# Performance work log

Measured on AMD Instinct MI355X. Metric: run time of the kernel, lower is better.

The kernel has to match this reference:

```python
import jax, jax.numpy as jnp
import numpy as np
from functools import partial

TAU = 2.0
BN_EPS = 1e-5
SG_ALPHA = 4.0  # spikingjelly surrogate.Sigmoid default

@jax.custom_vjp
def heaviside(x):
    return (x >= 0.0).astype(x.dtype)

def _heaviside_fwd(x):
    return heaviside(x), x

def _heaviside_bwd(x, g):
    s = jax.nn.sigmoid(SG_ALPHA * x)
    return (g * SG_ALPHA * s * (1.0 - s),)

heaviside.defvjp(_heaviside_fwd, _heaviside_bwd)

def lif(x_seq, v_threshold=1.0):
    # MultiStepLIFNode: tau=2, decay_input=True, v_reset=0 (hard reset), detach_reset
    def step(v, x):
        v = v + (x - v) / TAU
        s = heaviside(v - v_threshold)
        v = v * (1.0 - jax.lax.stop_gradient(s))
        return v, s
    _, s_seq = jax.lax.scan(step, jnp.zeros_like(x_seq[0]), x_seq)
    return s_seq

def conv1x1_bn(x, w, gamma, beta, mean, var, b=None):
    # x: [T,B,C,N]; w: [Cout,Cin]; 1x1 conv == channel matmul; BN in eval mode
    y = jnp.einsum('oc,tbcn->tbon', w, x)
    if b is not None:
        y = y + b[:, None]
    inv = gamma / jnp.sqrt(var + BN_EPS)
    return y * inv[:, None] + (beta - mean * inv)[:, None]

def setup_inputs() -> dict:
    key = jax.random.key(0)
    ks = jax.random.split(key, 24)
    T, B, C, N = 4, 32, 384, 196
    d = {}
    d['x'] = jax.random.normal(ks[0], (T, B, C, N), dtype=jnp.float32)
    d['policy'] = jax.random.uniform(ks[1], (T * B, N, 1), dtype=jnp.float32)
    scale = 1.0 / np.sqrt(C)
    for i, p in enumerate(['q', 'k', 'v', 'proj']):
        base = 2 + i * 5
        d[p + '_w'] = jax.random.normal(ks[base], (C, C), dtype=jnp.float32) * scale
        d[p + '_gamma'] = jnp.ones((C,), jnp.float32)
        d[p + '_beta'] = jnp.zeros((C,), jnp.float32)
        d[p + '_mean'] = jax.random.normal(ks[base + 1], (C,), dtype=jnp.float32) * 0.1
        d[p + '_var'] = jax.random.uniform(ks[base + 2], (C,), dtype=jnp.float32, minval=0.5, maxval=1.5)
    d['proj_b'] = jnp.zeros((C,), jnp.float32)
    return d

def _to_heads(s, H):
    T, B, C, N = s.shape
    # [T,B,C,N] -> [T,B,N,H,D] -> [T,B,H,N,D]
    return s.transpose(0, 1, 3, 2).reshape(T, B, N, H, C // H).transpose(0, 1, 3, 2, 4)

def reference(x, policy, q_w, q_gamma, q_beta, q_mean, q_var,
              k_w, k_gamma, k_beta, k_mean, k_var,
              v_w, v_gamma, v_beta, v_mean, v_var,
              proj_w, proj_gamma, proj_beta, proj_mean, proj_var, proj_b):
    T, B, C, N = x.shape
    H = 12
    attn_scale = 0.25
    q = _to_heads(lif(conv1x1_bn(x, q_w, q_gamma, q_beta, q_mean, q_var)), H)
    k = _to_heads(lif(conv1x1_bn(x, k_w, k_gamma, k_beta, k_mean, k_var)), H)
    v = _to_heads(lif(conv1x1_bn(x, v_w, v_gamma, v_beta, v_mean, v_var)), H)
    attn = jnp.einsum('tbhnd,tbhmd->tbhnm', q, k)
    # attention_policy: attn *= (policy + (1-policy)*eye)
    pol = policy.reshape(T, B, 1, 1, N)
    eye = jnp.eye(N, dtype=attn.dtype)
    attn = attn * (pol + (1.0 - pol) * eye)
    y = jnp.einsum('tbhnm,tbhmd->tbhnd', attn, v) * attn_scale
    y = y.transpose(0, 1, 2, 4, 3).reshape(T, B, C, N)
    y = lif(y, v_threshold=0.5)
    y = conv1x1_bn(y, proj_w, proj_gamma, proj_beta, proj_mean, proj_var, b=proj_b)
    return lif(y)
```

## Files before the change

### kernel.cpp

```cpp
#include <hip/hip_runtime.h>

typedef unsigned int u32;
typedef __bf16 bf16x8 __attribute__((ext_vector_type(8)));
typedef __bf16 bf16x4v __attribute__((ext_vector_type(4)));
typedef _Float16 f16x8 __attribute__((ext_vector_type(8)));
typedef float f32x4 __attribute__((ext_vector_type(4)));

#define Tn 4
#define Bn 32
#define Cn 384
#define Nn 196
#define Hn 12
#define CNn (Cn*Nn)
#define BCNn (Bn*CNn)
#define BHNn (Bn*Hn*Nn)
#define PBITS (Tn*BHNn)
#define TBCNn (Tn*BCNn)
#define NCOLS 6272
#define WSZ 147456

__device__ __forceinline__ void split3(float v, __bf16& h, __bf16& m, __bf16& l) {
  h = (__bf16)v;  float r = v - (float)h;
  m = (__bf16)r;  float r2 = r - (float)m;
  l = (__bf16)r2;
}
__device__ __forceinline__ void split2h(float v, _Float16& h, _Float16& l) {
  h = (_Float16)v;  l = (_Float16)(v - (float)h);
}

__device__ __forceinline__ void gl_lds16(const void* g, void* l) {
  __builtin_amdgcn_global_load_lds(
      (const __attribute__((address_space(1))) unsigned int*)g,
      (__attribute__((address_space(3))) unsigned int*)l, 16, 0, 0);
}

struct WSplitArgs {
  const float* w[4]; const float* g[4]; const float* be[4];
  const float* mu[4]; const float* va[4]; const float* bias;
};
__global__ __launch_bounds__(256) void prep(
    WSplitArgs a, _Float16* __restrict__ wsp16, __bf16* __restrict__ wspb,
    float* __restrict__ shv, const float* __restrict__ x,
    _Float16* __restrict__ xs) {
  __shared__ float tile[49 * 130];
  const int bx = blockIdx.x;
  const int tid = threadIdx.x;
  if (bx < 2304) {
    const int i = bx * 256 + tid;
    const int p = i / WSZ, r = i - p * WSZ;
    const int o = r / Cn, cc = r - o * Cn;
    const float iv = a.g[p][o] / sqrtf(a.va[p][o] + 1e-5f);
    const float wv = a.w[p][r] * iv;
    const int toff = ((o >> 4) * 12 + (cc >> 5)) * 512 +
                     (((cc >> 3) & 3) << 7) + ((o & 15) << 3) + (cc & 7);
    if (p < 3) {
      _Float16 h, l;
      split2h(wv, h, l);
      wsp16[(size_t)(p * 2 + 0) * WSZ + toff] = h;
      wsp16[(size_t)(p * 2 + 1) * WSZ + toff] = l;
    } else {
      __bf16 h, m, l;
      split3(wv, h, m, l);
      wspb[(size_t)0 * WSZ + toff] = h;
      wspb[(size_t)1 * WSZ + toff] = m;
      wspb[(size_t)2 * WSZ + toff] = l;
    }
    if (cc == 0) {
      float sh = a.be[p][o] - a.mu[p][o] * iv;
      if (p == 3) sh += a.bias[o] * iv;
      shv[p * Cn + o] = sh;
    }
    return;
  }
  const int bid2 = bx - 2304;
  const int t = bid2 & 3, b = (bid2 >> 2) & 31, zz = bid2 >> 7;
  const int ct = zz >> 2, nch = zz & 3;
  const int c0 = ct * 128, n0 = nch * 49;
  for (int idx = tid; idx < 49 * 128; idx += 256) {
    const int n = idx % 49, c = idx / 49;
    tile[n * 130 + c] = x[(size_t)t * BCNn + (size_t)b * CNn +
                          (size_t)(c0 + c) * Nn + n0 + n];
  }
  __syncthreads();
  for (int idx = tid; idx < 49 * 64; idx += 256) {
    const int cp = idx & 63, n = idx >> 6;
    const float v0 = tile[n * 130 + cp * 2];
    const float v1 = tile[n * 130 + cp * 2 + 1];
    _Float16 h0, l0, h1, l1;
    split2h(v0, h0, l0);
    split2h(v1, h1, l1);
    const size_t col = (size_t)t * NCOLS + (size_t)b * Nn + n0 + n;
    union { _Float16 f[2]; u32 u; } uh, ul;
    uh.f[0] = h0; uh.f[1] = h1;
    ul.f[0] = l0; ul.f[1] = l1;
    ((u32*)(xs + col * Cn + c0))[cp] = uh.u;
    ((u32*)(xs + (size_t)TBCNn + col * Cn + c0))[cp] = ul.u;
  }
}

__global__ __launch_bounds__(256, 2) void gemm_qkv_lif(
    const _Float16* __restrict__ xs,
    const _Float16* __restrict__ wsp16,
    const float* __restrict__ shv,
    u32* __restrict__ bq, u32* __restrict__ bk, u32* __restrict__ bv)
{
  __shared__ _Float16 Bsw[5][2][64][32];
  const int orig = blockIdx.x;
  const int xcd = orig & 7, i8 = orig >> 3;
  const int wgid = xcd * 110 + (xcd < 2 ? xcd : 2) + i8;
  const int colt = wgid / 9, v = wgid - colt * 9;
  const int col0 = colt * 64;
  const int p = v / 3, mt = v - p * 3;
  const int o0 = mt * 128;
  const int tid = threadIdx.x, lane = tid & 63, wid = tid >> 6;
  const int wm = wid >> 1, wn = wid & 1;
  const int quad = lane >> 4, nl = lane & 15;
  u32* __restrict__ bits = (p == 0) ? bq : (p == 1) ? bk : bv;

  u32 afOff[2][4];
#pragma unroll
  for (int s = 0; s < 2; ++s)
#pragma unroll
    for (int mi = 0; mi < 4; ++mi)
      afOff[s][mi] = (u32)((((p * 2 + s) * WSZ) +
                            (mt * 8 + wm * 4 + mi) * 6144) * 2) +
                     (u32)(lane * 16);
  u32 bOff[2];
#pragma unroll
  for (int i = 0; i < 2; ++i) {
    const int c = i * 256 + wid * 64 + lane;
    const int s = c >> 8, rem = c & 255, row = rem >> 2, kb = rem & 3;
    const int kbs = kb ^ ((row >> 1) & 3);
    bOff[i] = (u32)(((size_t)s * TBCNn + (size_t)(col0 + row) * Cn + kbs * 8) * 2);
  }
  const char* wB = (const char*)wsp16;
  const char* xB = (const char*)xs;
  char* bD0 = (char*)&Bsw[0][0][0][0] + wid * 1024;

#define STAGE_B(g_) do {                                                   \
    const int t_ = ((g_) / 24) * 2 + ((g_) & 1);                           \
    const int kk_ = (((g_) % 24) >> 1);                                    \
    const u32 bk_ = (u32)(kk_ * 64) + (u32)t_ * (u32)(NCOLS * Cn * 2);     \
    char* d_ = bD0 + ((g_) % 5) * 8192;                                    \
    _Pragma("unroll") for (int i_ = 0; i_ < 2; ++i_)                       \
      gl_lds16(xB + bOff[i_] + bk_, d_ + i_ * 4096);                       \
  } while (0)
#define LOAD_AF(DST, g_) do {                                              \
    const u32 ak2_ = (u32)(((g_) % 12) * 1024);                            \
    _Pragma("unroll") for (int s_ = 0; s_ < 2; ++s_)                       \
    _Pragma("unroll") for (int m_ = 0; m_ < 4; ++m_)                       \
      DST[s_][m_] = *(const f16x8*)(wB + afOff[s_][m_] + ak2_);            \
  } while (0)

  f32x4 sh_[4];
#pragma unroll
  for (int mi = 0; mi < 4; ++mi)
    sh_[mi] = *(const f32x4*)&shv[p * Cn + o0 + wm * 64 + mi * 16 + quad * 4];

  f32x4 acc0[4][2], acc1[4][2];
  f32x4 vst[4][2] = {};
  f16x8 afA[2][4], afB[2][4];

  auto epi = [&](f32x4 (&ac)[4][2], int t) {
#pragma unroll
    for (int ni = 0; ni < 2; ++ni) {
      u32 w0 = 0, w1 = 0;
#pragma unroll
      for (int mi = 0; mi < 4; ++mi) {
#pragma unroll
        for (int r = 0; r < 4; ++r) {
          const float y = ac[mi][ni][r] + sh_[mi][r];
          const float vv = vst[mi][ni][r];
          const float nv = vv + (y - vv) * 0.5f;
          const bool sk = nv >= 1.0f;
          vst[mi][ni][r] = sk ? 0.f : nv;
          const u32 b1 = sk ? 1u : 0u;
          const int pos = ((mi & 1) << 4) + (quad << 2) + r;
          if (mi < 2) w0 |= b1 << pos; else w1 |= b1 << pos;
        }
      }
      w0 |= __shfl_xor(w0, 16); w0 |= __shfl_xor(w0, 32);
      w1 |= __shfl_xor(w1, 16); w1 |= __shfl_xor(w1, 32);
      if (quad == 0) {
        const int col = col0 + wn * 32 + ni * 16 + nl;
        const int bb = col / Nn, nn = col - bb * Nn;
        u32* bp = bits + (size_t)t * BHNn +
                  ((size_t)bb * Hn + (mt * 4 + wm * 2)) * Nn + nn;
        bp[0] = w0;
        bp[Nn] = w1;
      }
    }
  };

  auto sub = [&](f16x8 (&afc)[2][4], f16x8 (&afn)[2][4], int g) {
    const int kk = g % 12;
    const int be = (2 * g) % 5, bo = (2 * g + 1) % 5;
    if (g == 0)       asm volatile("s_waitcnt vmcnt(14)" ::: "memory");
    else if (g == 23) asm volatile("s_waitcnt vmcnt(18)" ::: "memory");
    else              asm volatile("s_waitcnt vmcnt(22)" ::: "memory");
    __builtin_amdgcn_s_barrier();
    __builtin_amdgcn_sched_barrier(0);
    if (g < 22) STAGE_B(2 * g + 4);
    __builtin_amdgcn_sched_barrier(0);
    if (kk == 0) {
#pragma unroll
      for (int mi = 0; mi < 4; ++mi)
#pragma unroll
        for (int ni = 0; ni < 2; ++ni) {
          acc0[mi][ni] = f32x4{0.f, 0.f, 0.f, 0.f};
          acc1[mi][ni] = f32x4{0.f, 0.f, 0.f, 0.f};
        }
    }
    {
      f16x8 bfr[2][2];
#pragma unroll
      for (int i = 0; i < 2; ++i) {
        const int rb = wn * 32 + i * 16 + nl;
        const int kb2 = (quad ^ ((rb >> 1) & 3)) * 8;
        bfr[0][i] = *(const f16x8*)&Bsw[be][0][rb][kb2];
        bfr[1][i] = *(const f16x8*)&Bsw[be][1][rb][kb2];
      }
      __builtin_amdgcn_s_setprio(1);
#pragma unroll
      for (int mi = 0; mi < 4; ++mi)
#pragma unroll
        for (int ni = 0; ni < 2; ++ni) {
          f32x4 c = acc0[mi][ni];
          c = __builtin_amdgcn_mfma_f32_16x16x32_f16(afc[0][mi], bfr[0][ni], c, 0, 0, 0);
          c = __builtin_amdgcn_mfma_f32_16x16x32_f16(afc[0][mi], bfr[1][ni], c, 0, 0, 0);
          c = __builtin_amdgcn_mfma_f32_16x16x32_f16(afc[1][mi], bfr[0][ni], c, 0, 0, 0);
          acc0[mi][ni] = c;
        }
      __builtin_amdgcn_s_setprio(0);
    }
    if (g == 22)      asm volatile("s_waitcnt vmcnt(12)" ::: "memory");
    else if (g == 23) asm volatile("s_waitcnt vmcnt(8)"  ::: "memory");
    else              asm volatile("s_waitcnt vmcnt(14)" ::: "memory");
    __builtin_amdgcn_s_barrier();
    __builtin_amdgcn_sched_barrier(0);
    if (g < 23) LOAD_AF(afn, g + 1);
    __builtin_amdgcn_sched_barrier(0);
    if (g < 22) STAGE_B(2 * g + 5);
    __builtin_amdgcn_sched_barrier(0);
    {
      f16x8 bfr[2][2];
#pragma unroll
      for (int i = 0; i < 2; ++i) {
        const int rb = wn * 32 + i * 16 + nl;
        const int kb2 = (quad ^ ((rb >> 1) & 3)) * 8;
        bfr[0][i] = *(const f16x8*)&Bsw[bo][0][rb][kb2];
        bfr[1][i] = *(const f16x8*)&Bsw[bo][1][rb][kb2];
      }
      __builtin_amdgcn_s_setprio(1);
#pragma unroll
      for (int mi = 0; mi < 4; ++mi)
#pragma unroll
        for (int ni = 0; ni < 2; ++ni) {
          f32x4 c = acc1[mi][ni];
          c = __builtin_amdgcn_mfma_f32_16x16x32_f16(afc[0][mi], bfr[0][ni], c, 0, 0, 0);
          c = __builtin_amdgcn_mfma_f32_16x16x32_f16(afc[0][mi], bfr[1][ni], c, 0, 0, 0);
          c = __builtin_amdgcn_mfma_f32_16x16x32_f16(afc[1][mi], bfr[0][ni], c, 0, 0, 0);
          acc1[mi][ni] = c;
        }
      __builtin_amdgcn_s_setprio(0);
    }
    if (kk == 11) {
      const int p2 = g / 12;
      epi(acc0, p2 * 2 + 0);
      epi(acc1, p2 * 2 + 1);
    }
  };

  STAGE_B(0); STAGE_B(1); STAGE_B(2);
  LOAD_AF(afA, 0);
  STAGE_B(3);

#pragma unroll 1
  for (int gp = 0; gp < 12; ++gp) {
    sub(afA, afB, 2 * gp);
    sub(afB, afA, 2 * gp + 1);
  }
#undef STAGE_B
#undef LOAD_AF
}

#define USTR 232
#define GSTR 40
__global__ __launch_bounds__(256, 2) void attn_lif(
    const u32* __restrict__ qb, const u32* __restrict__ kb,
    const u32* __restrict__ vb, const float* __restrict__ policy,
    __bf16* __restrict__ sp) {
  __shared__ u32 qs[208], ks[224], vs_[224];
  __shared__ float ps[224];
  __shared__ __bf16 psp[3][224];
  __shared__ __bf16 Ul[3][32][USTR];
  __shared__ __bf16 GT[3][32][GSTR];
  const int bh = blockIdx.x;
  const int bN = bh / Hn;
  const int h = bh - bN * Hn;
  const int tid = threadIdx.x;
  const int lane = tid & 63, wid = tid >> 6;
  const int quad = lane >> 4, nl = lane & 15;
  const int wm1 = wid >> 1, wn1 = wid & 1;
  const __bf16 one = (__bf16)1.0f, zero = (__bf16)0.0f;

  float vst[4][2][4] = {};

  for (int t = 0; t < Tn; ++t) {
    const int tb = t * Bn + bN;
    const int gid = tb * Hn + h;
    if (t) __syncthreads();
    for (int i = tid; i < 224; i += 256) {
      const bool in = i < Nn;
      if (i < 208) qs[i] = in ? qb[(size_t)gid * Nn + i] : 0u;
      ks[i] = in ? kb[(size_t)gid * Nn + i] : 0u;
      vs_[i] = in ? vb[(size_t)gid * Nn + i] : 0u;
      const float p = in ? policy[(size_t)tb * Nn + i] : 0.f;
      ps[i] = p;
      __bf16 hh, mm, ll;
      split3(p, hh, mm, ll);
      psp[0][i] = hh; psp[1][i] = mm; psp[2][i] = ll;
    }
    __syncthreads();

#pragma unroll
    for (int it = 0; it < 7; ++it) {
      const int idx = tid + it * 256;
      const int d = idx & 31, mg = idx >> 5;
      __bf16 u4[3][4];
#pragma unroll
      for (int j = 0; j < 4; ++j) {
        const int m = mg * 4 + j;
        const bool bit = (vs_[m] >> d) & 1u;
#pragma unroll
        for (int s = 0; s < 3; ++s)
          u4[s][j] = bit ? psp[s][m] : zero;
      }
#pragma unroll
      for (int s = 0; s < 3; ++s)
        *(bf16x4v*)&Ul[s][d][mg * 4] = *(bf16x4v*)u4[s];
    }
    __syncthreads();

    f32x4 gacc = {0.f, 0.f, 0.f, 0.f};
    const int crow = wm1 * 16 + nl;
    const int drow = wn1 * 16 + nl;
#pragma unroll
    for (int slab = 0; slab < 7; ++slab) {
      const int m0 = slab * 32 + quad * 8;
      u32 kw[8];
      *(uint4*)&kw[0] = *(const uint4*)&ks[m0];
      *(uint4*)&kw[4] = *(const uint4*)&ks[m0 + 4];
      __bf16 a8[8];
#pragma unroll
      for (int j = 0; j < 8; ++j)
        a8[j] = ((kw[j] >> crow) & 1u) ? one : zero;
      const bf16x8 af = *(const bf16x8*)a8;
#pragma unroll
      for (int s = 0; s < 3; ++s)
        gacc = __builtin_amdgcn_mfma_f32_16x16x32_bf16(
            af, *(const bf16x8*)&Ul[s][drow][slab * 32 + quad * 8], gacc, 0, 0, 0);
    }
#pragma unroll
    for (int r = 0; r < 4; ++r) {
      __bf16 gh, gm, gl;
      split3(gacc[r], gh, gm, gl);
      const int cc = wm1 * 16 + quad * 4 + r;
      GT[0][drow][cc] = gh;
      GT[1][drow][cc] = gm;
      GT[2][drow][cc] = gl;
    }
    __syncthreads();

    bf16x8 bfr2[3][2];
#pragma unroll
    for (int s = 0; s < 3; ++s)
#pragma unroll
      for (int nt = 0; nt < 2; ++nt)
        bfr2[s][nt] = *(const bf16x8*)&GT[s][nt * 16 + nl][quad * 8];

    f32x4 acc2[4][2] = {};
#pragma unroll
    for (int mi = 0; mi < 4; ++mi) {
      const int lt = wid + mi * 4;
      if (lt < 13) {
        const u32 qw = qs[lt * 16 + nl];
        __bf16 a8[8];
#pragma unroll
        for (int j = 0; j < 8; ++j)
          a8[j] = ((qw >> (quad * 8 + j)) & 1u) ? one : zero;
        const bf16x8 af2 = *(const bf16x8*)a8;
#pragma unroll
        for (int nt = 0; nt < 2; ++nt) {
          f32x4 c = acc2[mi][nt];
          c = __builtin_amdgcn_mfma_f32_16x16x32_bf16(af2, bfr2[0][nt], c, 0, 0, 0);
          c = __builtin_amdgcn_mfma_f32_16x16x32_bf16(af2, bfr2[1][nt], c, 0, 0, 0);
          c = __builtin_amdgcn_mfma_f32_16x16x32_bf16(af2, bfr2[2][nt], c, 0, 0, 0);
          acc2[mi][nt] = c;
        }
      }
    }
#pragma unroll
    for (int mi = 0; mi < 4; ++mi) {
      const int lt = wid + mi * 4;
      if (lt >= 13) continue;
#pragma unroll
      for (int r = 0; r < 4; ++r) {
        const int n = lt * 16 + quad * 4 + r;
        if (n >= Nn) continue;
        const float ann = (float)__popc(qs[n] & ks[n]);
        const float wd = ann * (1.0f - ps[n]);
        const u32 vn = vs_[n];
        __bf16* op = sp + (size_t)t * BCNn + ((size_t)bN * Nn + n) * Cn + h * 32;
#pragma unroll
        for (int nt = 0; nt < 2; ++nt) {
          const int d = nt * 16 + nl;
          const float bit = (float)((vn >> d) & 1u);
          const float y = (acc2[mi][nt][r] + wd * bit) * 0.25f;
          const float vv = vst[mi][nt][r];
          const float nv = vv + (y - vv) * 0.5f;
          const bool s = nv >= 0.5f;
          vst[mi][nt][r] = s ? 0.f : nv;
          op[d] = (__bf16)(s ? 1.0f : 0.0f);
        }
      }
    }
  }
}

__global__ __launch_bounds__(256, 3) void gemm_proj_lif(
    const __bf16* __restrict__ sp, const __bf16* __restrict__ wspb,
    const float* __restrict__ shv, float* __restrict__ out)
{
  __shared__ __bf16 Bsw[5][64][32];
  const int orig = blockIdx.x;
  const int xcd = orig & 7, i8 = orig >> 3;
  const int wgid = xcd * 73 + (xcd < 4 ? xcd : 4) + i8;
  const int colt = wgid / 6, ot = wgid - colt * 6;
  const int col0 = colt * 64;
  const int o0 = ot * 64;
  const int tid = threadIdx.x, lane = tid & 63, wid = tid >> 6;
  const int wm = wid >> 1, wn = wid & 1;
  const int quad = lane >> 4, nl = lane & 15;

  u32 afOff[3][2];
#pragma unroll
  for (int s = 0; s < 3; ++s)
#pragma unroll
    for (int mi = 0; mi < 2; ++mi)
      afOff[s][mi] = (u32)(((s * WSZ) + (ot * 4 + wm * 2 + mi) * 6144) * 2) +
                     (u32)(lane * 16);
  u32 bOff;
  {
    const int c = wid * 64 + lane;
    const int row = c >> 2, kb = c & 3;
    const int kbs = kb ^ ((row >> 1) & 3);
    bOff = (u32)(((size_t)(col0 + row) * Cn + kbs * 8) * 2);
  }
  const char* wB = (const char*)wspb;
  const char* sB = (const char*)sp;
  char* bD0 = (char*)&Bsw[0][0][0] + wid * 1024;

#define STAGE_B(g_) do {                                                   \
    const int t_ = ((g_) / 24) * 2 + ((g_) & 1);                           \
    const int kk_ = (((g_) % 24) >> 1);                                    \
    const u32 bk_ = (u32)(kk_ * 64) + (u32)t_ * (u32)(BCNn * 2);           \
    gl_lds16(sB + bOff + bk_, bD0 + ((g_) % 5) * 4096);                    \
  } while (0)
#define LOAD_AF(DST, g_) do {                                              \
    const u32 ak2_ = (u32)(((g_) % 12) * 1024);                            \
    _Pragma("unroll") for (int s_ = 0; s_ < 3; ++s_)                       \
    _Pragma("unroll") for (int m_ = 0; m_ < 2; ++m_)                       \
      DST[s_][m_] = *(const bf16x8*)(wB + afOff[s_][m_] + ak2_);           \
  } while (0)

  f32x4 sh_[2];
#pragma unroll
  for (int mi = 0; mi < 2; ++mi)
    sh_[mi] = *(const f32x4*)&shv[3 * Cn + o0 + wm * 32 + mi * 16 + quad * 4];

  f32x4 acc0[2][2], acc1[2][2];
  f32x4 vst[2][2] = {};
  bf16x8 afA[3][2], afB[3][2];

  auto epi = [&](f32x4 (&ac)[2][2], int t) {
#pragma unroll
    for (int mi = 0; mi < 2; ++mi) {
      const int ob = o0 + wm * 32 + mi * 16 + quad * 4;
#pragma unroll
      for (int ni = 0; ni < 2; ++ni) {
        const int col = col0 + wn * 32 + ni * 16 + nl;
        const int bb = col / Nn, nn = col - bb * Nn;
        float* op = out + (size_t)t * BCNn + (size_t)bb * CNn + nn;
#pragma unroll
        for (int r = 0; r < 4; ++r) {
          const float y = ac[mi][ni][r] + sh_[mi][r];
          const float vv = vst[mi][ni][r];
          const float nv = vv + (y - vv) * 0.5f;
          const bool sk = nv >= 1.0f;
          vst[mi][ni][r] = sk ? 0.f : nv;
          op[(size_t)(ob + r) * Nn] = sk ? 1.0f : 0.0f;
        }
      }
    }
  };

  auto sub = [&](bf16x8 (&afc)[3][2], bf16x8 (&afn)[3][2], int g) {
    const int kk = g % 12;
    const int be = (2 * g) % 5, bo = (2 * g + 1) % 5;
    if (g == 23) asm volatile("s_waitcnt vmcnt(0)" ::: "memory");
    else         asm volatile("s_waitcnt vmcnt(1)" ::: "memory");
    __builtin_amdgcn_s_barrier();
    __builtin_amdgcn_sched_barrier(0);
    if (g < 22) STAGE_B(2 * g + 4);
    __builtin_amdgcn_sched_barrier(0);
    if (kk == 0) {
#pragma unroll
      for (int mi = 0; mi < 2; ++mi)
#pragma unroll
        for (int ni = 0; ni < 2; ++ni) {
          acc0[mi][ni] = f32x4{0.f, 0.f, 0.f, 0.f};
          acc1[mi][ni] = f32x4{0.f, 0.f, 0.f, 0.f};
        }
    }
    {
      bf16x8 bfr[2];
#pragma unroll
      for (int ni = 0; ni < 2; ++ni) {
        const int rb = wn * 32 + ni * 16 + nl;
        const int kb2 = (quad ^ ((rb >> 1) & 3)) * 8;
        bfr[ni] = *(const bf16x8*)&Bsw[be][rb][kb2];
      }
      __builtin_amdgcn_s_setprio(1);
#pragma unroll
      for (int mi = 0; mi < 2; ++mi)
#pragma unroll
        for (int ni = 0; ni < 2; ++ni) {
          f32x4 c = acc0[mi][ni];
          c = __builtin_amdgcn_mfma_f32_16x16x32_bf16(afc[0][mi], bfr[ni], c, 0, 0, 0);
          c = __builtin_amdgcn_mfma_f32_16x16x32_bf16(afc[1][mi], bfr[ni], c, 0, 0, 0);
          c = __builtin_amdgcn_mfma_f32_16x16x32_bf16(afc[2][mi], bfr[ni], c, 0, 0, 0);
          acc0[mi][ni] = c;
        }
      __builtin_amdgcn_s_setprio(0);
    }
    if (g == 22)      asm volatile("s_waitcnt vmcnt(1)" ::: "memory");
    else if (g == 23) asm volatile("s_waitcnt vmcnt(0)" ::: "memory");
    else              asm volatile("s_waitcnt vmcnt(2)" ::: "memory");
    __builtin_amdgcn_s_barrier();
    __builtin_amdgcn_sched_barrier(0);
    if (g < 23) LOAD_AF(afn, g + 1);
    __builtin_amdgcn_sched_barrier(0);
    if (g < 22) STAGE_B(2 * g + 5);
    __builtin_amdgcn_sched_barrier(0);
    {
      bf16x8 bfr[2];
#pragma unroll
      for (int ni = 0; ni < 2; ++ni) {
        const int rb = wn * 32 + ni * 16 + nl;
        const int kb2 = (quad ^ ((rb >> 1) & 3)) * 8;
        bfr[ni] = *(const bf16x8*)&Bsw[bo][rb][kb2];
      }
      __builtin_amdgcn_s_setprio(1);
#pragma unroll
      for (int mi = 0; mi < 2; ++mi)
#pragma unroll
        for (int ni = 0; ni < 2; ++ni) {
          f32x4 c = acc1[mi][ni];
          c = __builtin_amdgcn_mfma_f32_16x16x32_bf16(afc[0][mi], bfr[ni], c, 0, 0, 0);
          c = __builtin_amdgcn_mfma_f32_16x16x32_bf16(afc[1][mi], bfr[ni], c, 0, 0, 0);
          c = __builtin_amdgcn_mfma_f32_16x16x32_bf16(afc[2][mi], bfr[ni], c, 0, 0, 0);
          acc1[mi][ni] = c;
        }
      __builtin_amdgcn_s_setprio(0);
    }
    if (kk == 11) {
      const int p2 = g / 12;
      epi(acc0, p2 * 2 + 0);
      epi(acc1, p2 * 2 + 1);
    }
  };

  STAGE_B(0); STAGE_B(1); STAGE_B(2);
  LOAD_AF(afA, 0);
  STAGE_B(3);

#pragma unroll 1
  for (int gp = 0; gp < 12; ++gp) {
    sub(afA, afB, 2 * gp);
    sub(afB, afA, 2 * gp + 1);
  }
#undef STAGE_B
#undef LOAD_AF
}

extern "C" void kernel_launch(void* const* d_in, const int* in_sizes, int n_in,
                              void* d_out, int out_size, void* d_ws, size_t ws_size,
                              hipStream_t stream) {
  const float* x      = (const float*)d_in[0];
  const float* policy = (const float*)d_in[1];
  const float* qw = (const float*)d_in[2];
  const float* qg = (const float*)d_in[3];
  const float* qb_ = (const float*)d_in[4];
  const float* qm = (const float*)d_in[5];
  const float* qv = (const float*)d_in[6];
  const float* kw = (const float*)d_in[7];
  const float* kg = (const float*)d_in[8];
  const float* kbe = (const float*)d_in[9];
  const float* km = (const float*)d_in[10];
  const float* kv = (const float*)d_in[11];
  const float* vw = (const float*)d_in[12];
  const float* vg = (const float*)d_in[13];
  const float* vbe = (const float*)d_in[14];
  const float* vm = (const float*)d_in[15];
  const float* vv = (const float*)d_in[16];
  const float* pw = (const float*)d_in[17];
  const float* pg = (const float*)d_in[18];
  const float* pbe = (const float*)d_in[19];
  const float* pm = (const float*)d_in[20];
  const float* pv = (const float*)d_in[21];
  const float* pbias = (const float*)d_in[22];
  float* out = (float*)d_out;

  char* base = (char*)d_ws;
  _Float16* xs   = (_Float16*)base;
  _Float16* wsp16 = (_Float16*)(base + (size_t)TBCNn * 4);
  __bf16* wspb   = (__bf16*)((char*)wsp16 + (size_t)6 * WSZ * 2);
  float* shv     = (float*)((char*)wspb + (size_t)3 * WSZ * 2);
  u32* bq        = (u32*)((char*)shv + 4 * Cn * 4);
  u32* bk = bq + PBITS;
  u32* bv = bk + PBITS;
  __bf16* sp     = (__bf16*)(bv + PBITS);

  WSplitArgs wa;
  wa.w[0] = qw; wa.g[0] = qg; wa.be[0] = qb_; wa.mu[0] = qm; wa.va[0] = qv;
  wa.w[1] = kw; wa.g[1] = kg; wa.be[1] = kbe; wa.mu[1] = km; wa.va[1] = kv;
  wa.w[2] = vw; wa.g[2] = vg; wa.be[2] = vbe; wa.mu[2] = vm; wa.va[2] = vv;
  wa.w[3] = pw; wa.g[3] = pg; wa.be[3] = pbe; wa.mu[3] = pm; wa.va[3] = pv;
  wa.bias = pbias;
  prep<<<3840, 256, 0, stream>>>(wa, wsp16, wspb, shv, x, xs);

  gemm_qkv_lif<<<882, 256, 0, stream>>>(xs, wsp16, shv, bq, bk, bv);
  attn_lif<<<Bn * Hn, 256, 0, stream>>>(bq, bk, bv, policy, sp);
  gemm_proj_lif<<<588, 256, 0, stream>>>(sp, wspb, shv, out);
}
```

Baseline: 274.1 us.

## Merge two half-steps into one barrier phase with six-slot LDS ring

```diff
diff --git a/kernel.cpp b/kernel.cpp
--- a/kernel.cpp
+++ b/kernel.cpp
@@ -104,7 +104,7 @@
     const float* __restrict__ shv,
     u32* __restrict__ bq, u32* __restrict__ bk, u32* __restrict__ bv)
 {
-  __shared__ _Float16 Bsw[5][2][64][32];
+  __shared__ _Float16 Bsw[6][2][64][32];
   const int orig = blockIdx.x;
   const int xcd = orig & 7, i8 = orig >> 3;
   const int wgid = xcd * 110 + (xcd < 2 ? xcd : 2) + i8;
@@ -141,7 +141,7 @@
     const int t_ = ((g_) / 24) * 2 + ((g_) & 1);                           \
     const int kk_ = (((g_) % 24) >> 1);                                    \
     const u32 bk_ = (u32)(kk_ * 64) + (u32)t_ * (u32)(NCOLS * Cn * 2);     \
-    char* d_ = bD0 + ((g_) % 5) * 8192;                                    \
+    char* d_ = bD0 + ((g_) % 6) * 8192;                                    \
     _Pragma("unroll") for (int i_ = 0; i_ < 2; ++i_)                       \
       gl_lds16(xB + bOff[i_] + bk_, d_ + i_ * 4096);                       \
   } while (0)
@@ -194,13 +194,14 @@
 
   auto sub = [&](f16x8 (&afc)[2][4], f16x8 (&afn)[2][4], int g) {
     const int kk = g % 12;
-    const int be = (2 * g) % 5, bo = (2 * g + 1) % 5;
-    if (g == 0)       asm volatile("s_waitcnt vmcnt(14)" ::: "memory");
-    else if (g == 23) asm volatile("s_waitcnt vmcnt(18)" ::: "memory");
-    else              asm volatile("s_waitcnt vmcnt(22)" ::: "memory");
+    const int be = (2 * g) % 6, bo = (2 * g + 1) % 6;
+    if (g == 23) asm volatile("s_waitcnt vmcnt(8)"  ::: "memory");
+    else         asm volatile("s_waitcnt vmcnt(12)" ::: "memory");
     __builtin_amdgcn_s_barrier();
     __builtin_amdgcn_sched_barrier(0);
     if (g < 22) STAGE_B(2 * g + 4);
+    if (g < 23) LOAD_AF(afn, g + 1);
+    if (g < 22) STAGE_B(2 * g + 5);
     __builtin_amdgcn_sched_barrier(0);
     if (kk == 0) {
 #pragma unroll
@@ -212,13 +213,15 @@
         }
     }
     {
-      f16x8 bfr[2][2];
+      f16x8 bfrE[2][2], bfrO[2][2];
 #pragma unroll
       for (int i = 0; i < 2; ++i) {
         const int rb = wn * 32 + i * 16 + nl;
         const int kb2 = (quad ^ ((rb >> 1) & 3)) * 8;
-        bfr[0][i] = *(const f16x8*)&Bsw[be][0][rb][kb2];
-        bfr[1][i] = *(const f16x8*)&Bsw[be][1][rb][kb2];
+        bfrE[0][i] = *(const f16x8*)&Bsw[be][0][rb][kb2];
+        bfrE[1][i] = *(const f16x8*)&Bsw[be][1][rb][kb2];
+        bfrO[0][i] = *(const f16x8*)&Bsw[bo][0][rb][kb2];
+        bfrO[1][i] = *(const f16x8*)&Bsw[bo][1][rb][kb2];
       }
       __builtin_amdgcn_s_setprio(1);
 #pragma unroll
@@ -226,41 +229,15 @@
 #pragma unroll
         for (int ni = 0; ni < 2; ++ni) {
           f32x4 c = acc0[mi][ni];
-          c = __builtin_amdgcn_mfma_f32_16x16x32_f16(afc[0][mi], bfr[0][ni], c, 0, 0, 0);
-          c = __builtin_amdgcn_mfma_f32_16x16x32_f16(afc[0][mi], bfr[1][ni], c, 0, 0, 0);
-          c = __builtin_amdgcn_mfma_f32_16x16x32_f16(afc[1][mi], bfr[0][ni], c, 0, 0, 0);
+          c = __builtin_amdgcn_mfma_f32_16x16x32_f16(afc[0][mi], bfrE[0][ni], c, 0, 0, 0);
+          c = __builtin_amdgcn_mfma_f32_16x16x32_f16(afc[0][mi], bfrE[1][ni], c, 0, 0, 0);
+          c = __builtin_amdgcn_mfma_f32_16x16x32_f16(afc[1][mi], bfrE[0][ni], c, 0, 0, 0);
           acc0[mi][ni] = c;
-        }
-      __builtin_amdgcn_s_setprio(0);
-    }
-    if (g == 22)      asm volatile("s_waitcnt vmcnt(12)" ::: "memory");
-    else if (g == 23) asm volatile("s_waitcnt vmcnt(8)"  ::: "memory");
-    else              asm volatile("s_waitcnt vmcnt(14)" ::: "memory");
-    __builtin_amdgcn_s_barrier();
-    __builtin_amdgcn_sched_barrier(0);
-    if (g < 23) LOAD_AF(afn, g + 1);
-    __builtin_amdgcn_sched_barrier(0);
-    if (g < 22) STAGE_B(2 * g + 5);
-    __builtin_amdgcn_sched_barrier(0);
-    {
-      f16x8 bfr[2][2];
-#pragma unroll
-      for (int i = 0; i < 2; ++i) {
-        const int rb = wn * 32 + i * 16 + nl;
-        const int kb2 = (quad ^ ((rb >> 1) & 3)) * 8;
-        bfr[0][i] = *(const f16x8*)&Bsw[bo][0][rb][kb2];
-        bfr[1][i] = *(const f16x8*)&Bsw[bo][1][rb][kb2];
-      }
-      __builtin_amdgcn_s_setprio(1);
-#pragma unroll
-      for (int mi = 0; mi < 4; ++mi)
-#pragma unroll
-        for (int ni = 0; ni < 2; ++ni) {
-          f32x4 c = acc1[mi][ni];
-          c = __builtin_amdgcn_mfma_f32_16x16x32_f16(afc[0][mi], bfr[0][ni], c, 0, 0, 0);
-          c = __builtin_amdgcn_mfma_f32_16x16x32_f16(afc[0][mi], bfr[1][ni], c, 0, 0, 0);
-          c = __builtin_amdgcn_mfma_f32_16x16x32_f16(afc[1][mi], bfr[0][ni], c, 0, 0, 0);
-          acc1[mi][ni] = c;
+          f32x4 d = acc1[mi][ni];
+          d = __builtin_amdgcn_mfma_f32_16x16x32_f16(afc[0][mi], bfrO[0][ni], d, 0, 0, 0);
+          d = __builtin_amdgcn_mfma_f32_16x16x32_f16(afc[0][mi], bfrO[1][ni], d, 0, 0, 0);
+          d = __builtin_amdgcn_mfma_f32_16x16x32_f16(afc[1][mi], bfrO[0][ni], d, 0, 0, 0);
+          acc1[mi][ni] = d;
         }
       __builtin_amdgcn_s_setprio(0);
     }
@@ -432,7 +409,7 @@
     const __bf16* __restrict__ sp, const __bf16* __restrict__ wspb,
     const float* __restrict__ shv, float* __restrict__ out)
 {
-  __shared__ __bf16 Bsw[5][64][32];
+  __shared__ __bf16 Bsw[6][64][32];
   const int orig = blockIdx.x;
   const int xcd = orig & 7, i8 = orig >> 3;
   const int wgid = xcd * 73 + (xcd < 4 ? xcd : 4) + i8;
@@ -465,7 +442,7 @@
     const int t_ = ((g_) / 24) * 2 + ((g_) & 1);                           \
     const int kk_ = (((g_) % 24) >> 1);                                    \
     const u32 bk_ = (u32)(kk_ * 64) + (u32)t_ * (u32)(BCNn * 2);           \
-    gl_lds16(sB + bOff + bk_, bD0 + ((g_) % 5) * 4096);                    \
+    gl_lds16(sB + bOff + bk_, bD0 + ((g_) % 6) * 4096);                    \
   } while (0)
 #define LOAD_AF(DST, g_) do {                                              \
     const u32 ak2_ = (u32)(((g_) % 12) * 1024);                            \
@@ -507,12 +484,14 @@
 
   auto sub = [&](bf16x8 (&afc)[3][2], bf16x8 (&afn)[3][2], int g) {
     const int kk = g % 12;
-    const int be = (2 * g) % 5, bo = (2 * g + 1) % 5;
-    if (g == 23) asm volatile("s_waitcnt vmcnt(0)" ::: "memory");
-    else         asm volatile("s_waitcnt vmcnt(1)" ::: "memory");
+    const int be = (2 * g) % 6, bo = (2 * g + 1) % 6;
+    if (g == 23) asm volatile("s_waitcnt vmcnt(6)" ::: "memory");
+    else         asm volatile("s_waitcnt vmcnt(8)" ::: "memory");
     __builtin_amdgcn_s_barrier();
     __builtin_amdgcn_sched_barrier(0);
     if (g < 22) STAGE_B(2 * g + 4);
+    if (g < 23) LOAD_AF(afn, g + 1);
+    if (g < 22) STAGE_B(2 * g + 5);
     __builtin_amdgcn_sched_barrier(0);
     if (kk == 0) {
 #pragma unroll
@@ -524,12 +503,13 @@
         }
     }
     {
-      bf16x8 bfr[2];
+      bf16x8 bfrE[2], bfrO[2];
 #pragma unroll
       for (int ni = 0; ni < 2; ++ni) {
         const int rb = wn * 32 + ni * 16 + nl;
         const int kb2 = (quad ^ ((rb >> 1) & 3)) * 8;
-        bfr[ni] = *(const bf16x8*)&Bsw[be][rb][kb2];
+        bfrE[ni] = *(const bf16x8*)&Bsw[be][rb][kb2];
+        bfrO[ni] = *(const bf16x8*)&Bsw[bo][rb][kb2];
       }
       __builtin_amdgcn_s_setprio(1);
 #pragma unroll
@@ -537,40 +517,15 @@
 #pragma unroll
         for (int ni = 0; ni < 2; ++ni) {
           f32x4 c = acc0[mi][ni];
-          c = __builtin_amdgcn_mfma_f32_16x16x32_bf16(afc[0][mi], bfr[ni], c, 0, 0, 0);
-          c = __builtin_amdgcn_mfma_f32_16x16x32_bf16(afc[1][mi], bfr[ni], c, 0, 0, 0);
-          c = __builtin_amdgcn_mfma_f32_16x16x32_bf16(afc[2][mi], bfr[ni], c, 0, 0, 0);
+          c = __builtin_amdgcn_mfma_f32_16x16x32_bf16(afc[0][mi], bfrE[ni], c, 0, 0, 0);
+          c = __builtin_amdgcn_mfma_f32_16x16x32_bf16(afc[1][mi], bfrE[ni], c, 0, 0, 0);
+          c = __builtin_amdgcn_mfma_f32_16x16x32_bf16(afc[2][mi], bfrE[ni], c, 0, 0, 0);
           acc0[mi][ni] = c;
-        }
-      __builtin_amdgcn_s_setprio(0);
-    }
-    if (g == 22)      asm volatile("s_waitcnt vmcnt(1)" ::: "memory");
-    else if (g == 23) asm volatile("s_waitcnt vmcnt(0)" ::: "memory");
-    else              asm volatile("s_waitcnt vmcnt(2)" ::: "memory");
-    __builtin_amdgcn_s_barrier();
-    __builtin_amdgcn_sched_barrier(0);
-    if (g < 23) LOAD_AF(afn, g + 1);
-    __builtin_amdgcn_sched_barrier(0);
-    if (g < 22) STAGE_B(2 * g + 5);
-    __builtin_amdgcn_sched_barrier(0);
-    {
-      bf16x8 bfr[2];
-#pragma unroll
-      for (int ni = 0; ni < 2; ++ni) {
-        const int rb = wn * 32 + ni * 16 + nl;
-        const int kb2 = (quad ^ ((rb >> 1) & 3)) * 8;
-        bfr[ni] = *(const bf16x8*)&Bsw[bo][rb][kb2];
-      }
-      __builtin_amdgcn_s_setprio(1);
-#pragma unroll
-      for (int mi = 0; mi < 2; ++mi)
-#pragma unroll
-        for (int ni = 0; ni < 2; ++ni) {
-          f32x4 c = acc1[mi][ni];
-          c = __builtin_amdgcn_mfma_f32_16x16x32_bf16(afc[0][mi], bfr[ni], c, 0, 0, 0);
-          c = __builtin_amdgcn_mfma_f32_16x16x32_bf16(afc[1][mi], bfr[ni], c, 0, 0, 0);
-          c = __builtin_amdgcn_mfma_f32_16x16x32_bf16(afc[2][mi], bfr[ni], c, 0, 0, 0);
-          acc1[mi][ni] = c;
+          f32x4 d = acc1[mi][ni];
+          d = __builtin_amdgcn_mfma_f32_16x16x32_bf16(afc[0][mi], bfrO[ni], d, 0, 0, 0);
+          d = __builtin_amdgcn_mfma_f32_16x16x32_bf16(afc[1][mi], bfrO[ni], d, 0, 0, 0);
+          d = __builtin_amdgcn_mfma_f32_16x16x32_bf16(afc[2][mi], bfrO[ni], d, 0, 0, 0);
+          acc1[mi][ni] = d;
         }
       __builtin_amdgcn_s_setprio(0);
     }
```

Measured after the change: 268.6 us. 1.02x faster.
